# Kernel optimization log

Measured on AMD Instinct MI355X. Metric: run time of the kernel, lower is better.

Reference implementation:

```python
import jax, jax.numpy as jnp
import numpy as np

B, T, D = 32, 512, 256
F = 256  # duration_predictor_filter_size
K = 3    # kernel size, padding=1
MEL_MAX = 2304
EPS = 1e-5


def _conv1d(x, w, b):
    # x: [B, T, C_in], w: [C_out, C_in, K], 'same'-ish padding=1
    y = jax.lax.conv_general_dilated(
        x.transpose(0, 2, 1), w, window_strides=(1,), padding=[(1, 1)],
        dimension_numbers=("NCH", "OIH", "NCH"))
    return y.transpose(0, 2, 1) + b


def _layernorm(x, g, b):
    mu = jnp.mean(x, axis=-1, keepdims=True)
    var = jnp.mean(jnp.square(x - mu), axis=-1, keepdims=True)
    return (x - mu) * jax.lax.rsqrt(var + EPS) * g + b


def setup_inputs() -> dict:
    key = jax.random.key(0)
    ks = jax.random.split(key, 8)
    x = jax.random.normal(ks[0], (B, T, D), dtype=jnp.float32)
    target = jax.random.randint(ks[1], (B, T), 0, 8, dtype=jnp.int32)
    s = 0.02
    return {
        "x": x,
        "target": target,
        "mel_max_length": MEL_MAX,
        "conv1_w": jax.random.normal(ks[2], (F, D, K), dtype=jnp.float32) * s,
        "conv1_b": jnp.zeros((F,), jnp.float32),
        "ln1_g": jnp.ones((F,), jnp.float32),
        "ln1_b": jnp.zeros((F,), jnp.float32),
        "conv2_w": jax.random.normal(ks[3], (F, F, K), dtype=jnp.float32) * s,
        "conv2_b": jnp.zeros((F,), jnp.float32),
        "ln2_g": jnp.ones((F,), jnp.float32),
        "ln2_b": jnp.zeros((F,), jnp.float32),
        "lin_w": jax.random.normal(ks[4], (1, F), dtype=jnp.float32) * s,
        "lin_b": jnp.zeros((1,), jnp.float32),
    }


def reference(x, target, mel_max_length, conv1_w, conv1_b, ln1_g, ln1_b,
              conv2_w, conv2_b, ln2_g, ln2_b, lin_w, lin_b):
    # Variance_adaptor (duration predictor), eval-mode dropout = identity
    h = jax.nn.relu(_layernorm(_conv1d(x, conv1_w, conv1_b), ln1_g, ln1_b))
    h = jax.nn.relu(_layernorm(_conv1d(h, conv2_w, conv2_b), ln2_g, ln2_b))
    dur_pred = jax.nn.relu(jnp.einsum("btf,of->bto", h, lin_w) + lin_b)[..., 0]  # [B,T]

    # LR: alignment @ x, expressed as the equivalent duration-indexed gather.
    # alignment[b, t_out, j] = 1 iff cumsum(dur)[b,j-1] <= t_out < cumsum(dur)[b,j]
    cum = jnp.cumsum(target, axis=1)                    # [B, T]
    t_out = jnp.arange(mel_max_length, dtype=cum.dtype)  # [T_out]
    idx = jax.vmap(lambda c: jnp.searchsorted(c, t_out, side="right"))(cum)  # [B, T_out]
    valid = (t_out[None, :] < cum[:, -1:]).astype(x.dtype)                   # [B, T_out]
    gathered = jnp.take_along_axis(x, jnp.clip(idx, 0, T - 1)[:, :, None], axis=1)
    output = gathered * valid[:, :, None]                # zeros past total length (pad)
    return output, dur_pred
```

## Files before the change

### kernel.cpp

```cpp
#include <hip/hip_runtime.h>

typedef __attribute__((ext_vector_type(8))) short short8;
typedef __attribute__((ext_vector_type(4))) float floatx4;

typedef __attribute__((address_space(3))) unsigned int lds_u32;
typedef __attribute__((address_space(1))) const unsigned int glb_u32;

static __device__ __forceinline__ unsigned short f2bf(float f) {
    unsigned int u = __float_as_uint(f);
    return (unsigned short)((u + 0x7FFFu + ((u >> 16) & 1u)) >> 16);
}
static __device__ __forceinline__ void cp16(const ushort* g, ushort* l) {
    __builtin_amdgcn_global_load_lds((glb_u32*)g, (lds_u32*)l, 16, 0, 0);
}

__global__ __launch_bounds__(256)
void prep_kernel(const float* __restrict__ x, const float* __restrict__ w1,
                 const float* __restrict__ w2,
                 ushort* __restrict__ xb, ushort* __restrict__ h1b,
                 ushort* __restrict__ w1pb, ushort* __restrict__ w2pb)
{
    const int blk = blockIdx.x, tid = threadIdx.x;
    if (blk < 4112) {
        const int r = blk * 4 + (tid >> 6);
        const int c = (tid & 63) * 4;
        const int b = r / 514, tp = r % 514;
        ushort4 o;
        if (tp >= 1 && tp <= 512) {
            float4 v = *(const float4*)(x + ((size_t)(b * 512 + tp - 1) * 256 + c));
            o.x = f2bf(v.x); o.y = f2bf(v.y); o.z = f2bf(v.z); o.w = f2bf(v.w);
        } else {
            o.x = o.y = o.z = o.w = 0;
            *(ushort4*)(h1b + (size_t)r * 256 + c) = o;
        }
        *(ushort4*)(xb + (size_t)r * 256 + c) = o;
    } else {
        const bool second = blk >= 4880;
        const int e = (blk - (second ? 4880 : 4112)) * 256 + tid;
        const float* w = second ? w2 : w1;
        ushort* wpb = second ? w2pb : w1pb;
        const int f = e / 768, j = e % 768;
        const int c = j & 255, kr = j >> 8;
        const int s = j >> 6, kk = j & 63;
        wpb[s * 16384 + f * 64 + (((kk >> 3) ^ (f & 7)) << 3) + (kk & 7)]
            = f2bf(w[f * 768 + c * 3 + kr]);
    }
}

template<bool IS_CONV2>
__global__ __launch_bounds__(256, 2)
void conv_mfma_kernel(const ushort* __restrict__ xb,
                      const ushort* __restrict__ wpb,
                      const float* __restrict__ cbias,
                      const float* __restrict__ gamma, const float* __restrict__ beta,
                      const float* __restrict__ lw, const float* __restrict__ lb,
                      ushort* __restrict__ outb,
                      float* __restrict__ durp,
                      const float* __restrict__ x,
                      const int* __restrict__ target,
                      float* __restrict__ out0)
{
    __shared__ ushort Bws[4][2][4096];
    __shared__ float sum_s[4][32], sq_s[4][32], mu_s[32], rs_s[32];
    __shared__ int cum[512], ps[256], sidx[64];

    const int tid = threadIdx.x;

    if (IS_CONV2 && blockIdx.x >= 512) {
        const int bg = blockIdx.x - 512;
        const int b = bg / 36, t0o = (bg % 36) * 64;
        const int v0 = target[b * 512 + 2 * tid];
        const int v1 = target[b * 512 + 2 * tid + 1];
        ps[tid] = v0 + v1;
        __syncthreads();
        for (int off = 1; off < 256; off <<= 1) {
            int t = (tid >= off) ? ps[tid - off] : 0;
            __syncthreads();
            ps[tid] += t;
            __syncthreads();
        }
        const int excl = tid ? ps[tid - 1] : 0;
        cum[2 * tid]     = excl + v0;
        cum[2 * tid + 1] = excl + v0 + v1;
        __syncthreads();
        const int total = cum[511];
        if (tid < 64) {
            int t = t0o + tid;
            int lo = 0, hi = 512;
            while (lo < hi) {
                int mid = (lo + hi) >> 1;
                if (cum[mid] <= t) lo = mid + 1; else hi = mid;
            }
            sidx[tid] = (t < total) ? ((lo < 512) ? lo : 511) : -1;
        }
        __syncthreads();
        const float4* x4 = (const float4*)x;
        float4* o4 = (float4*)out0;
        const int lane6 = tid & 63, g4 = tid >> 6;
        #pragma unroll 4
        for (int rr = 0; rr < 16; ++rr) {
            int r = rr * 4 + g4;
            int idx = sidx[r];
            float4 v = make_float4(0.f, 0.f, 0.f, 0.f);
            if (idx >= 0) v = x4[((size_t)(b * 512 + idx)) * 64 + lane6];
            o4[((size_t)(b * 2304 + t0o + r)) * 64 + lane6] = v;
        }
        return;
    }

    const int w_ = tid >> 6, lane = tid & 63;
    const int q = lane >> 4, col = lane & 15;
    const int b  = blockIdx.x >> 4;
    const int t0 = (blockIdx.x & 15) << 5;

    floatx4 acc[2][4] = {};
    const ushort* xbb = xb + ((size_t)b * 514 + t0) * 256;
    const ushort* wpw = wpb + w_ * 4096 + lane * 8;
    ushort* buf0 = &Bws[w_][0][0];
    ushort* buf1 = &Bws[w_][1][0];

    short8 afb[2][2][2];

    #pragma unroll
    for (int i = 0; i < 8; ++i) cp16(wpw + i * 512, buf0 + i * 512);
    #pragma unroll
    for (int mi = 0; mi < 2; ++mi)
        #pragma unroll
        for (int kh = 0; kh < 2; ++kh)
            afb[0][mi][kh] = *(const short8*)(xbb + (size_t)(mi * 16 + col) * 256
                                              + kh * 32 + q * 8);

    #pragma unroll
    for (int s = 0; s < 12; ++s) {
        const int sp = (s < 11) ? s + 1 : 11;
        const int krow = sp >> 2, cb = (sp & 3) << 6;
        ushort* nbuf = (s & 1) ? buf0 : buf1;
        const ushort* wsrc = wpw + (size_t)sp * 16384;
        #pragma unroll
        for (int i = 0; i < 8; ++i) cp16(wsrc + i * 512, nbuf + i * 512);
        #pragma unroll
        for (int mi = 0; mi < 2; ++mi)
            #pragma unroll
            for (int kh = 0; kh < 2; ++kh)
                afb[(s + 1) & 1][mi][kh] = *(const short8*)(xbb
                    + (size_t)(mi * 16 + col + krow) * 256 + cb + kh * 32 + q * 8);
        asm volatile("s_waitcnt vmcnt(12)" ::: "memory");
        const ushort* cbuf = (s & 1) ? buf1 : buf0;
        short8 bfr[4][2];
        #pragma unroll
        for (int ni = 0; ni < 4; ++ni)
            #pragma unroll
            for (int kh = 0; kh < 2; ++kh)
                bfr[ni][kh] = *(const short8*)((const char*)cbuf
                    + (ni * 16 + col) * 128 + (((kh * 4 + q) ^ (col & 7)) << 4));
        #pragma unroll
        for (int kh = 0; kh < 2; ++kh)
            #pragma unroll
            for (int mi = 0; mi < 2; ++mi)
                #pragma unroll
                for (int ni = 0; ni < 4; ++ni)
                    acc[mi][ni] = __builtin_amdgcn_mfma_f32_16x16x32_bf16(
                        afb[s & 1][mi][kh], bfr[ni][kh], acc[mi][ni], 0, 0, 0);
    }

    const int base_c = w_ * 64;
    float cb4[4], gm4[4], bt4[4];
    #pragma unroll
    for (int ni = 0; ni < 4; ++ni) {
        cb4[ni] = cbias[base_c + ni * 16 + col];
        gm4[ni] = gamma[base_c + ni * 16 + col];
        bt4[ni] = beta [base_c + ni * 16 + col];
    }
    float rsum[2][4] = {}, rsq[2][4] = {};
    #pragma unroll
    for (int mi = 0; mi < 2; ++mi)
        #pragma unroll
        for (int ni = 0; ni < 4; ++ni)
            #pragma unroll
            for (int r = 0; r < 4; ++r) {
                float v = acc[mi][ni][r] + cb4[ni];
                acc[mi][ni][r] = v;
                rsum[mi][r] += v;
                rsq [mi][r] += v * v;
            }
    #pragma unroll
    for (int mi = 0; mi < 2; ++mi)
        #pragma unroll
        for (int r = 0; r < 4; ++r) {
            float s = rsum[mi][r], ss = rsq[mi][r];
            #pragma unroll
            for (int d = 8; d > 0; d >>= 1) {
                s  += __shfl_down(s,  d, 16);
                ss += __shfl_down(ss, d, 16);
            }
            if (col == 0) {
                sum_s[w_][mi * 16 + q * 4 + r] = s;
                sq_s [w_][mi * 16 + q * 4 + r] = ss;
            }
        }
    __syncthreads();
    if (tid < 32) {
        float s  = sum_s[0][tid] + sum_s[1][tid] + sum_s[2][tid] + sum_s[3][tid];
        float ss = sq_s [0][tid] + sq_s [1][tid] + sq_s [2][tid] + sq_s [3][tid];
        float mu = s * (1.f / 256.f);
        mu_s[tid] = mu;
        rs_s[tid] = rsqrtf(ss * (1.f / 256.f) - mu * mu + 1e-5f);
    }
    __syncthreads();

    if (!IS_CONV2) {
        #pragma unroll
        for (int mi = 0; mi < 2; ++mi)
            #pragma unroll
            for (int ni = 0; ni < 4; ++ni)
                #pragma unroll
                for (int r = 0; r < 4; ++r) {
                    int row = mi * 16 + q * 4 + r;
                    float v = (acc[mi][ni][r] - mu_s[row]) * rs_s[row] * gm4[ni] + bt4[ni];
                    outb[((size_t)b * 514 + t0 + row + 1) * 256 + base_c + ni * 16 + col]
                        = f2bf(fmaxf(v, 0.f));
                }
    } else {
        float lw4[4];
        #pragma unroll
        for (int ni = 0; ni < 4; ++ni) lw4[ni] = lw[base_c + ni * 16 + col];
        float dsum[2][4] = {};
        #pragma unroll
        for (int mi = 0; mi < 2; ++mi)
            #pragma unroll
            for (int ni = 0; ni < 4; ++ni)
                #pragma unroll
                for (int r = 0; r < 4; ++r) {
                    int row = mi * 16 + q * 4 + r;
                    float v = (acc[mi][ni][r] - mu_s[row]) * rs_s[row] * gm4[ni] + bt4[ni];
                    dsum[mi][r] += fmaxf(v, 0.f) * lw4[ni];
                }
        #pragma unroll
        for (int mi = 0; mi < 2; ++mi)
            #pragma unroll
            for (int r = 0; r < 4; ++r) {
                float s = dsum[mi][r];
                #pragma unroll
                for (int d = 8; d > 0; d >>= 1) s += __shfl_down(s, d, 16);
                if (col == 0) sum_s[w_][mi * 16 + q * 4 + r] = s;
            }
        __syncthreads();
        if (tid < 32)
            durp[b * 512 + t0 + tid] = fmaxf(sum_s[0][tid] + sum_s[1][tid]
                                           + sum_s[2][tid] + sum_s[3][tid] + lb[0], 0.f);
    }
}

extern "C" void kernel_launch(void* const* d_in, const int* in_sizes, int n_in,
                              void* d_out, int out_size, void* d_ws, size_t ws_size,
                              hipStream_t stream) {
    const float* x      = (const float*)d_in[0];
    const int*   target = (const int*)  d_in[1];
    const float* c1w = (const float*)d_in[3];
    const float* c1b = (const float*)d_in[4];
    const float* g1  = (const float*)d_in[5];
    const float* b1  = (const float*)d_in[6];
    const float* c2w = (const float*)d_in[7];
    const float* c2b = (const float*)d_in[8];
    const float* g2  = (const float*)d_in[9];
    const float* b2  = (const float*)d_in[10];
    const float* lw  = (const float*)d_in[11];
    const float* lb  = (const float*)d_in[12];

    const size_t PADEL = (size_t)32 * 514 * 256;
    ushort* xb   = (ushort*)d_ws;
    ushort* h1b  = xb + PADEL;
    ushort* w1pb = h1b + PADEL;
    ushort* w2pb = w1pb + 196608;

    float* out0 = (float*)d_out;
    float* durp = out0 + (size_t)32 * 2304 * 256;

    prep_kernel<<<5648, 256, 0, stream>>>(x, c1w, c2w, xb, h1b, w1pb, w2pb);
    conv_mfma_kernel<false><<<512, 256, 0, stream>>>(
        xb, w1pb, c1b, g1, b1, nullptr, nullptr, h1b, nullptr,
        nullptr, nullptr, nullptr);
    conv_mfma_kernel<true><<<512 + 1152, 256, 0, stream>>>(
        h1b, w2pb, c2b, g2, b2, lw, lb, nullptr, durp,
        x, target, out0);
}
```

Before: 168.6 us.

## Stage activation tile in LDS and share weight stages across 8-wave blocks

The conv kernels now use 512-thread blocks covering 64 time rows, loading the full padded input tile (66 rows) into swizzled LDS once. Weights stream in 24 K-stages through a 4-deep LDS ring shared by all waves, synchronized with barriers. Before, each wave held a private copy of the weights and loaded activations straight from global memory. The gather blocks are also resized to 128 output rows with a 512-wide scan. This cuts redundant weight traffic, but it halves the grid to 256 conv blocks on a large-CU GPU and adds a barrier on every stage.

```diff
diff --git a/kernel.cpp b/kernel.cpp
--- a/kernel.cpp
+++ b/kernel.cpp
@@ -40,16 +40,17 @@
         const float* w = second ? w2 : w1;
         ushort* wpb = second ? w2pb : w1pb;
         const int f = e / 768, j = e % 768;
-        const int c = j & 255, kr = j >> 8;
-        const int s = j >> 6, kk = j & 63;
-        wpb[s * 16384 + f * 64 + (((kk >> 3) ^ (f & 7)) << 3) + (kk & 7)]
-            = f2bf(w[f * 768 + c * 3 + kr]);
+        const int s = j >> 5, kk = j & 31;
+        const int jd = kk >> 3, o = kk & 7;
+        const int jsrc = s * 32 + (jd ^ ((f >> 1) & 3)) * 8 + o;
+        const int c = jsrc & 255, kr = jsrc >> 8;
+        wpb[s * 8192 + f * 32 + kk] = f2bf(w[f * 768 + c * 3 + kr]);
     }
 }
 
 template<bool IS_CONV2>
-__global__ __launch_bounds__(256, 2)
-void conv_mfma_kernel(const ushort* __restrict__ xb,
+__global__ __launch_bounds__(512, 2)
+void conv_mfma_kernel(const ushort* __restrict__ inb_g,
                       const ushort* __restrict__ wpb,
                       const float* __restrict__ cbias,
                       const float* __restrict__ gamma, const float* __restrict__ beta,
@@ -60,32 +61,27 @@
                       const int* __restrict__ target,
                       float* __restrict__ out0)
 {
-    __shared__ ushort Bws[4][2][4096];
-    __shared__ float sum_s[4][32], sq_s[4][32], mu_s[32], rs_s[32];
-    __shared__ int cum[512], ps[256], sidx[64];
+    __shared__ ushort As[66 * 256];
+    __shared__ ushort Bs[4 * 8192];
+    __shared__ float sum_s[8][64], sq_s[8][64], mu_s[64], rs_s[64];
+    __shared__ int cum[512], sidx[128];
 
     const int tid = threadIdx.x;
 
-    if (IS_CONV2 && blockIdx.x >= 512) {
-        const int bg = blockIdx.x - 512;
-        const int b = bg / 36, t0o = (bg % 36) * 64;
-        const int v0 = target[b * 512 + 2 * tid];
-        const int v1 = target[b * 512 + 2 * tid + 1];
-        ps[tid] = v0 + v1;
+    if (IS_CONV2 && blockIdx.x >= 256) {
+        const int g = blockIdx.x - 256;
+        const int b = g / 18, seg = g % 18;
+        cum[tid] = target[b * 512 + tid];
         __syncthreads();
-        for (int off = 1; off < 256; off <<= 1) {
-            int t = (tid >= off) ? ps[tid - off] : 0;
+        for (int off = 1; off < 512; off <<= 1) {
+            int v = (tid >= off) ? cum[tid - off] : 0;
             __syncthreads();
-            ps[tid] += t;
+            cum[tid] += v;
             __syncthreads();
         }
-        const int excl = tid ? ps[tid - 1] : 0;
-        cum[2 * tid]     = excl + v0;
-        cum[2 * tid + 1] = excl + v0 + v1;
-        __syncthreads();
         const int total = cum[511];
-        if (tid < 64) {
-            int t = t0o + tid;
+        if (tid < 128) {
+            int t = seg * 128 + tid;
             int lo = 0, hi = 512;
             while (lo < hi) {
                 int mid = (lo + hi) >> 1;
@@ -96,95 +92,108 @@
         __syncthreads();
         const float4* x4 = (const float4*)x;
         float4* o4 = (float4*)out0;
-        const int lane6 = tid & 63, g4 = tid >> 6;
+        const int lane6 = tid & 63, g8 = tid >> 6;
         #pragma unroll 4
-        for (int rr = 0; rr < 16; ++rr) {
-            int r = rr * 4 + g4;
+        for (int it = 0; it < 16; ++it) {
+            int r = it * 8 + g8;
             int idx = sidx[r];
             float4 v = make_float4(0.f, 0.f, 0.f, 0.f);
             if (idx >= 0) v = x4[((size_t)(b * 512 + idx)) * 64 + lane6];
-            o4[((size_t)(b * 2304 + t0o + r)) * 64 + lane6] = v;
+            o4[((size_t)(b * 2304 + seg * 128 + r)) * 64 + lane6] = v;
         }
         return;
     }
 
     const int w_ = tid >> 6, lane = tid & 63;
     const int q = lane >> 4, col = lane & 15;
-    const int b  = blockIdx.x >> 4;
-    const int t0 = (blockIdx.x & 15) << 5;
-
-    floatx4 acc[2][4] = {};
-    const ushort* xbb = xb + ((size_t)b * 514 + t0) * 256;
-    const ushort* wpw = wpb + w_ * 4096 + lane * 8;
-    ushort* buf0 = &Bws[w_][0][0];
-    ushort* buf1 = &Bws[w_][1][0];
-
-    short8 afb[2][2][2];
-
-    #pragma unroll
-    for (int i = 0; i < 8; ++i) cp16(wpw + i * 512, buf0 + i * 512);
-    #pragma unroll
-    for (int mi = 0; mi < 2; ++mi)
-        #pragma unroll
-        for (int kh = 0; kh < 2; ++kh)
-            afb[0][mi][kh] = *(const short8*)(xbb + (size_t)(mi * 16 + col) * 256
-                                              + kh * 32 + q * 8);
-
-    #pragma unroll
-    for (int s = 0; s < 12; ++s) {
-        const int sp = (s < 11) ? s + 1 : 11;
-        const int krow = sp >> 2, cb = (sp & 3) << 6;
-        ushort* nbuf = (s & 1) ? buf0 : buf1;
-        const ushort* wsrc = wpw + (size_t)sp * 16384;
-        #pragma unroll
-        for (int i = 0; i < 8; ++i) cp16(wsrc + i * 512, nbuf + i * 512);
-        #pragma unroll
-        for (int mi = 0; mi < 2; ++mi)
-            #pragma unroll
-            for (int kh = 0; kh < 2; ++kh)
-                afb[(s + 1) & 1][mi][kh] = *(const short8*)(xbb
-                    + (size_t)(mi * 16 + col + krow) * 256 + cb + kh * 32 + q * 8);
-        asm volatile("s_waitcnt vmcnt(12)" ::: "memory");
-        const ushort* cbuf = (s & 1) ? buf1 : buf0;
-        short8 bfr[4][2];
-        #pragma unroll
-        for (int ni = 0; ni < 4; ++ni)
-            #pragma unroll
-            for (int kh = 0; kh < 2; ++kh)
-                bfr[ni][kh] = *(const short8*)((const char*)cbuf
-                    + (ni * 16 + col) * 128 + (((kh * 4 + q) ^ (col & 7)) << 4));
-        #pragma unroll
-        for (int kh = 0; kh < 2; ++kh)
-            #pragma unroll
-            for (int mi = 0; mi < 2; ++mi)
-                #pragma unroll
-                for (int ni = 0; ni < 4; ++ni)
-                    acc[mi][ni] = __builtin_amdgcn_mfma_f32_16x16x32_bf16(
-                        afb[s & 1][mi][kh], bfr[ni][kh], acc[mi][ni], 0, 0, 0);
-    }
-
-    const int base_c = w_ * 64;
-    float cb4[4], gm4[4], bt4[4];
-    #pragma unroll
-    for (int ni = 0; ni < 4; ++ni) {
-        cb4[ni] = cbias[base_c + ni * 16 + col];
-        gm4[ni] = gamma[base_c + ni * 16 + col];
-        bt4[ni] = beta [base_c + ni * 16 + col];
-    }
-    float rsum[2][4] = {}, rsq[2][4] = {};
-    #pragma unroll
-    for (int mi = 0; mi < 2; ++mi)
-        #pragma unroll
-        for (int ni = 0; ni < 4; ++ni)
+    const int b  = blockIdx.x >> 3;
+    const int t0 = (blockIdx.x & 7) << 6;
+
+    const ushort* inB = inb_g + (size_t)b * 514 * 256;
+
+    #pragma unroll
+    for (int i = 0; i < 4; ++i) {
+        const int ch = w_ + i * 8;
+        const int ri = 2 * ch + (lane >> 5);
+        const int jd = lane & 31;
+        const int js = (jd & 24) | ((jd & 7) ^ (ri & 7));
+        cp16(inB + (size_t)(t0 + ri) * 256 + js * 8, As + ch * 512);
+    }
+    if (w_ == 0) {
+        const int ri = 64 + (lane >> 5);
+        const int jd = lane & 31;
+        const int js = (jd & 24) | ((jd & 7) ^ (ri & 7));
+        cp16(inB + (size_t)(t0 + ri) * 256 + js * 8, As + 32 * 512);
+    }
+    #pragma unroll
+    for (int s = 0; s < 2; ++s)
+        #pragma unroll
+        for (int i = 0; i < 2; ++i)
+            cp16(wpb + s * 8192 + i * 4096 + w_ * 512 + lane * 8,
+                 Bs + s * 8192 + i * 4096 + w_ * 512);
+
+    floatx4 acc[4][2] = {};
+
+    #pragma unroll
+    for (int s = 0; s < 24; ++s) {
+        if (s < 23) asm volatile("s_waitcnt vmcnt(2)" ::: "memory");
+        else        asm volatile("s_waitcnt vmcnt(0)" ::: "memory");
+        __builtin_amdgcn_s_barrier();
+
+        const int krow = s >> 3, kb = s & 7;
+        const ushort* bb = Bs + (s & 3) * 8192;
+        short8 af[4], bf[2];
+        #pragma unroll
+        for (int mi = 0; mi < 4; ++mi) {
+            const int ri = mi * 16 + col + krow;
+            const int jq = kb * 4 + q;
+            const int js = (jq & 24) | ((jq & 7) ^ (ri & 7));
+            af[mi] = *(const short8*)(As + ri * 256 + js * 8);
+        }
+        #pragma unroll
+        for (int ni = 0; ni < 2; ++ni) {
+            const int brow = w_ * 32 + ni * 16 + col;
+            const int jd = q ^ ((brow >> 1) & 3);
+            bf[ni] = *(const short8*)(bb + brow * 32 + jd * 8);
+        }
+        if (s + 2 < 24) {
+            const int sp = s + 2;
+            #pragma unroll
+            for (int i = 0; i < 2; ++i)
+                cp16(wpb + sp * 8192 + i * 4096 + w_ * 512 + lane * 8,
+                     Bs + (sp & 3) * 8192 + i * 4096 + w_ * 512);
+        }
+        #pragma unroll
+        for (int mi = 0; mi < 4; ++mi)
+            #pragma unroll
+            for (int ni = 0; ni < 2; ++ni)
+                acc[mi][ni] = __builtin_amdgcn_mfma_f32_16x16x32_bf16(
+                    af[mi], bf[ni], acc[mi][ni], 0, 0, 0);
+    }
+    __syncthreads();
+
+    const int bc0 = w_ * 32;
+    float cb2[2], gm2[2], bt2[2];
+    #pragma unroll
+    for (int ni = 0; ni < 2; ++ni) {
+        cb2[ni] = cbias[bc0 + ni * 16 + col];
+        gm2[ni] = gamma[bc0 + ni * 16 + col];
+        bt2[ni] = beta [bc0 + ni * 16 + col];
+    }
+    float rsum[4][4] = {}, rsq[4][4] = {};
+    #pragma unroll
+    for (int mi = 0; mi < 4; ++mi)
+        #pragma unroll
+        for (int ni = 0; ni < 2; ++ni)
             #pragma unroll
             for (int r = 0; r < 4; ++r) {
-                float v = acc[mi][ni][r] + cb4[ni];
+                float v = acc[mi][ni][r] + cb2[ni];
                 acc[mi][ni][r] = v;
                 rsum[mi][r] += v;
                 rsq [mi][r] += v * v;
             }
     #pragma unroll
-    for (int mi = 0; mi < 2; ++mi)
+    for (int mi = 0; mi < 4; ++mi)
         #pragma unroll
         for (int r = 0; r < 4; ++r) {
             float s = rsum[mi][r], ss = rsq[mi][r];
@@ -199,9 +208,10 @@
             }
         }
     __syncthreads();
-    if (tid < 32) {
-        float s  = sum_s[0][tid] + sum_s[1][tid] + sum_s[2][tid] + sum_s[3][tid];
-        float ss = sq_s [0][tid] + sq_s [1][tid] + sq_s [2][tid] + sq_s [3][tid];
+    if (tid < 64) {
+        float s = 0.f, ss = 0.f;
+        #pragma unroll
+        for (int wv = 0; wv < 8; ++wv) { s += sum_s[wv][tid]; ss += sq_s[wv][tid]; }
         float mu = s * (1.f / 256.f);
         mu_s[tid] = mu;
         rs_s[tid] = rsqrtf(ss * (1.f / 256.f) - mu * mu + 1e-5f);
@@ -210,33 +220,33 @@
 
     if (!IS_CONV2) {
         #pragma unroll
-        for (int mi = 0; mi < 2; ++mi)
-            #pragma unroll
-            for (int ni = 0; ni < 4; ++ni)
+        for (int mi = 0; mi < 4; ++mi)
+            #pragma unroll
+            for (int ni = 0; ni < 2; ++ni)
                 #pragma unroll
                 for (int r = 0; r < 4; ++r) {
-                    int row = mi * 16 + q * 4 + r;
-                    float v = (acc[mi][ni][r] - mu_s[row]) * rs_s[row] * gm4[ni] + bt4[ni];
-                    outb[((size_t)b * 514 + t0 + row + 1) * 256 + base_c + ni * 16 + col]
+                    const int row = mi * 16 + q * 4 + r;
+                    float v = (acc[mi][ni][r] - mu_s[row]) * rs_s[row] * gm2[ni] + bt2[ni];
+                    outb[((size_t)b * 514 + t0 + row + 1) * 256 + bc0 + ni * 16 + col]
                         = f2bf(fmaxf(v, 0.f));
                 }
     } else {
-        float lw4[4];
-        #pragma unroll
-        for (int ni = 0; ni < 4; ++ni) lw4[ni] = lw[base_c + ni * 16 + col];
-        float dsum[2][4] = {};
-        #pragma unroll
-        for (int mi = 0; mi < 2; ++mi)
-            #pragma unroll
-            for (int ni = 0; ni < 4; ++ni)
+        float lw2[2];
+        #pragma unroll
+        for (int ni = 0; ni < 2; ++ni) lw2[ni] = lw[bc0 + ni * 16 + col];
+        float dsum[4][4] = {};
+        #pragma unroll
+        for (int mi = 0; mi < 4; ++mi)
+            #pragma unroll
+            for (int ni = 0; ni < 2; ++ni)
                 #pragma unroll
                 for (int r = 0; r < 4; ++r) {
-                    int row = mi * 16 + q * 4 + r;
-                    float v = (acc[mi][ni][r] - mu_s[row]) * rs_s[row] * gm4[ni] + bt4[ni];
-                    dsum[mi][r] += fmaxf(v, 0.f) * lw4[ni];
+                    const int row = mi * 16 + q * 4 + r;
+                    float v = (acc[mi][ni][r] - mu_s[row]) * rs_s[row] * gm2[ni] + bt2[ni];
+                    dsum[mi][r] += fmaxf(v, 0.f) * lw2[ni];
                 }
         #pragma unroll
-        for (int mi = 0; mi < 2; ++mi)
+        for (int mi = 0; mi < 4; ++mi)
             #pragma unroll
             for (int r = 0; r < 4; ++r) {
                 float s = dsum[mi][r];
@@ -245,9 +255,12 @@
                 if (col == 0) sum_s[w_][mi * 16 + q * 4 + r] = s;
             }
         __syncthreads();
-        if (tid < 32)
-            durp[b * 512 + t0 + tid] = fmaxf(sum_s[0][tid] + sum_s[1][tid]
-                                           + sum_s[2][tid] + sum_s[3][tid] + lb[0], 0.f);
+        if (tid < 64) {
+            float s = 0.f;
+            #pragma unroll
+            for (int wv = 0; wv < 8; ++wv) s += sum_s[wv][tid];
+            durp[b * 512 + t0 + tid] = fmaxf(s + lb[0], 0.f);
+        }
     }
 }
 
@@ -277,10 +290,10 @@
     float* durp = out0 + (size_t)32 * 2304 * 256;
 
     prep_kernel<<<5648, 256, 0, stream>>>(x, c1w, c2w, xb, h1b, w1pb, w2pb);
-    conv_mfma_kernel<false><<<512, 256, 0, stream>>>(
+    conv_mfma_kernel<false><<<256, 512, 0, stream>>>(
         xb, w1pb, c1b, g1, b1, nullptr, nullptr, h1b, nullptr,
         nullptr, nullptr, nullptr);
-    conv_mfma_kernel<true><<<512 + 1152, 256, 0, stream>>>(
+    conv_mfma_kernel<true><<<256 + 576, 512, 0, stream>>>(
         h1b, w2pb, c2b, g2, b2, lw, lb, nullptr, durp,
         x, target, out0);
 }
```

New measurement: 157.8 us. -6.4%, faster.
